# Kernel optimization log

Measured on AMD Instinct MI355X. Metric: run time of the kernel, lower is better.

## Reference

```python
import jax, jax.numpy as jnp
import numpy as np

# Each of the 16 real-valued binary logic gates g_i(a,b) is multilinear in (a,b):
# g_i(a,b) = c0 + c1*a + c2*b + c3*a*b. Rows below are [c0, c1, c2, c3] for gates 0..15
# (false, a&b, a&~b, a, ~a&b, b, xor, or, nor, xnor, ~b, a|~b, ~a, ~a|b, nand, true).
_GATE_COEFFS = np.array([
    [0.0,  0.0,  0.0,  0.0],   # 0: False
    [0.0,  0.0,  0.0,  1.0],   # 1: a AND b
    [0.0,  1.0,  0.0, -1.0],   # 2: a AND NOT b
    [0.0,  1.0,  0.0,  0.0],   # 3: a
    [0.0,  0.0,  1.0, -1.0],   # 4: NOT a AND b
    [0.0,  0.0,  1.0,  0.0],   # 5: b
    [0.0,  1.0,  1.0, -2.0],   # 6: a XOR b
    [0.0,  1.0,  1.0, -1.0],   # 7: a OR b
    [1.0, -1.0, -1.0,  1.0],   # 8: NOR
    [1.0, -1.0, -1.0,  2.0],   # 9: XNOR
    [1.0,  0.0, -1.0,  0.0],   # 10: NOT b
    [1.0,  0.0, -1.0,  1.0],   # 11: a OR NOT b
    [1.0, -1.0,  0.0,  0.0],   # 12: NOT a
    [1.0, -1.0,  0.0,  1.0],   # 13: NOT a OR b
    [1.0,  0.0,  0.0, -1.0],   # 14: NAND
    [1.0,  0.0,  0.0,  0.0],   # 15: True
], dtype=np.float32)

BATCH, IN_DIM, OUT_DIM = 4096, 16384, 16384

def setup_inputs() -> dict:
    key = jax.random.key(0)
    k1, k2, k3, k4 = jax.random.split(key, 4)
    x = jax.random.uniform(k1, (BATCH, IN_DIM), dtype=jnp.float32)
    weights = jax.random.normal(k2, (OUT_DIM, 16), dtype=jnp.float32)
    # get_connections('random'): randperm(2*out_dim) % in_dim -> uniform indices in [0, in_dim)
    a_idx = jax.random.randint(k3, (OUT_DIM,), 0, IN_DIM, dtype=jnp.int64)
    b_idx = jax.random.randint(k4, (OUT_DIM,), 0, IN_DIM, dtype=jnp.int64)
    return {"x": x, "weights": weights, "a_idx": a_idx, "b_idx": b_idx}

def reference(x, weights, a_idx, b_idx):
    # softmax over the 16 gate logits (per output neuron)
    w = jax.nn.softmax(weights, axis=-1).astype(x.dtype)          # [out, 16]
    # collapse 16 gates into 4 multilinear coefficients: k = w @ M  -> [out, 4]
    k = w @ jnp.asarray(_GATE_COEFFS, dtype=x.dtype)
    a = x[:, a_idx]                                               # [batch, out] gather
    b = x[:, b_idx]                                               # [batch, out] gather
    # out[n, y] = k0[y] + k1[y]*a + k2[y]*b + k3[y]*a*b
    return k[:, 0] + k[:, 1] * a + k[:, 2] * b + k[:, 3] * (a * b)
```

## Files before the change

kernel.cpp:

```cpp
#include <hip/hip_runtime.h>


__device__ __constant__ float GC[16][4] = {
    {0.f, 0.f, 0.f, 0.f},  {0.f, 0.f, 0.f, 1.f},
    {0.f, 1.f, 0.f, -1.f}, {0.f, 1.f, 0.f, 0.f},
    {0.f, 0.f, 1.f, -1.f}, {0.f, 0.f, 1.f, 0.f},
    {0.f, 1.f, 1.f, -2.f}, {0.f, 1.f, 1.f, -1.f},
    {1.f, -1.f, -1.f, 1.f},{1.f, -1.f, -1.f, 2.f},
    {1.f, 0.f, -1.f, 0.f}, {1.f, 0.f, -1.f, 1.f},
    {1.f, -1.f, 0.f, 0.f}, {1.f, -1.f, 0.f, 1.f},
    {1.f, 0.f, 0.f, -1.f}, {1.f, 0.f, 0.f, 0.f}};

__global__ void meta_kernel(const float* __restrict__ weights,
                            const int* __restrict__ a_idx,
                            const int* __restrict__ b_idx,
                            float4* __restrict__ k_out,
                            int2* __restrict__ idx_out, int out_dim) {
    int c = blockIdx.x * blockDim.x + threadIdx.x;
    if (c >= out_dim) return;
    const float4* wr = (const float4*)(weights + (size_t)c * 16);
    float4 q0 = wr[0], q1 = wr[1], q2 = wr[2], q3 = wr[3];
    float w[16] = {q0.x, q0.y, q0.z, q0.w, q1.x, q1.y, q1.z, q1.w,
                   q2.x, q2.y, q2.z, q2.w, q3.x, q3.y, q3.z, q3.w};
    float m = w[0];
#pragma unroll
    for (int i = 1; i < 16; ++i) m = fmaxf(m, w[i]);
    float S = 0.f, s0 = 0.f, s1 = 0.f, s2 = 0.f, s3 = 0.f;
#pragma unroll
    for (int i = 0; i < 16; ++i) {
        float e = expf(w[i] - m);
        S += e;
        s0 = fmaf(e, GC[i][0], s0);
        s1 = fmaf(e, GC[i][1], s1);
        s2 = fmaf(e, GC[i][2], s2);
        s3 = fmaf(e, GC[i][3], s3);
    }
    float inv = 1.f / S;
    k_out[c] = make_float4(s0 * inv, s1 * inv, s2 * inv, s3 * inv);
    idx_out[c] = make_int2(a_idx[c], b_idx[c]);
}

__global__ __launch_bounds__(512) void logic_main_kernel(
    const float* __restrict__ x, const float4* __restrict__ k_meta,
    const int2* __restrict__ idx_meta, float* __restrict__ out,
    int in_dim, int out_dim) {
    __shared__ float rowbuf[16384];
    const int row = blockIdx.x;
    const float4* src = (const float4*)(x + (size_t)row * in_dim);
    float4* dst = (float4*)rowbuf;
    const int n4in = in_dim >> 2;
    for (int i = threadIdx.x; i < n4in; i += 512) dst[i] = src[i];
    __syncthreads();

    float4* orow = (float4*)(out + (size_t)row * out_dim);
    const int n4out = out_dim >> 2;
    for (int q = threadIdx.x; q < n4out; q += 512) {
        const int c = q << 2;
        int2 ab0 = idx_meta[c + 0];
        int2 ab1 = idx_meta[c + 1];
        int2 ab2 = idx_meta[c + 2];
        int2 ab3 = idx_meta[c + 3];
        float4 k0 = k_meta[c + 0];
        float4 k1 = k_meta[c + 1];
        float4 k2 = k_meta[c + 2];
        float4 k3 = k_meta[c + 3];
        float a0 = rowbuf[ab0.x], b0 = rowbuf[ab0.y];
        float a1 = rowbuf[ab1.x], b1 = rowbuf[ab1.y];
        float a2 = rowbuf[ab2.x], b2 = rowbuf[ab2.y];
        float a3 = rowbuf[ab3.x], b3 = rowbuf[ab3.y];
        float4 r;
        r.x = fmaf(k0.w, a0 * b0, fmaf(k0.z, b0, fmaf(k0.y, a0, k0.x)));
        r.y = fmaf(k1.w, a1 * b1, fmaf(k1.z, b1, fmaf(k1.y, a1, k1.x)));
        r.z = fmaf(k2.w, a2 * b2, fmaf(k2.z, b2, fmaf(k2.y, a2, k2.x)));
        r.w = fmaf(k3.w, a3 * b3, fmaf(k3.z, b3, fmaf(k3.y, a3, k3.x)));
        orow[q] = r;
    }
}

__global__ void fallback_kernel(const float* __restrict__ x,
                                const float* __restrict__ weights,
                                const int* __restrict__ a_idx,
                                const int* __restrict__ b_idx,
                                float* __restrict__ out, long long total,
                                int in_dim, int out_dim) {
    long long stride = (long long)gridDim.x * blockDim.x;
    for (long long t = (long long)blockIdx.x * blockDim.x + threadIdx.x;
         t < total; t += stride) {
        int c = (int)(t % out_dim);
        long long row = t / out_dim;
        const float* wr = weights + (size_t)c * 16;
        float m = wr[0];
#pragma unroll
        for (int i = 1; i < 16; ++i) m = fmaxf(m, wr[i]);
        float S = 0.f, s0 = 0.f, s1 = 0.f, s2 = 0.f, s3 = 0.f;
#pragma unroll
        for (int i = 0; i < 16; ++i) {
            float e = expf(wr[i] - m);
            S += e;
            s0 = fmaf(e, GC[i][0], s0);
            s1 = fmaf(e, GC[i][1], s1);
            s2 = fmaf(e, GC[i][2], s2);
            s3 = fmaf(e, GC[i][3], s3);
        }
        float inv = 1.f / S;
        float a = x[row * (size_t)in_dim + a_idx[c]];
        float b = x[row * (size_t)in_dim + b_idx[c]];
        out[t] = fmaf(s3 * inv, a * b,
                      fmaf(s2 * inv, b, fmaf(s1 * inv, a, s0 * inv)));
    }
}

extern "C" void kernel_launch(void* const* d_in, const int* in_sizes, int n_in,
                              void* d_out, int out_size, void* d_ws,
                              size_t ws_size, hipStream_t stream) {
    const float* x = (const float*)d_in[0];
    const float* weights = (const float*)d_in[1];
    const int* a_idx = (const int*)d_in[2];
    const int* b_idx = (const int*)d_in[3];
    float* out = (float*)d_out;

    const int out_dim = in_sizes[2];
    const int batch = out_size / out_dim;
    const int in_dim = in_sizes[0] / batch;

    const size_t k_bytes = (size_t)out_dim * sizeof(float4);
    const size_t idx_bytes = (size_t)out_dim * sizeof(int2);

    const bool ok = ws_size >= k_bytes + idx_bytes && in_dim <= 16384 &&
                    (in_dim % 4) == 0 && (out_dim % 4) == 0;
    if (ok) {
        float4* k_meta = (float4*)d_ws;
        int2* idx_meta = (int2*)((char*)d_ws + k_bytes);
        meta_kernel<<<(out_dim + 255) / 256, 256, 0, stream>>>(
            weights, a_idx, b_idx, k_meta, idx_meta, out_dim);
        logic_main_kernel<<<batch, 512, 0, stream>>>(x, k_meta, idx_meta, out,
                                                     in_dim, out_dim);
    } else {
        long long total = (long long)batch * out_dim;
        fallback_kernel<<<4096, 256, 0, stream>>>(x, weights, a_idx, b_idx,
                                                  out, total, in_dim, out_dim);
    }
}
```

Before: 540.7 us.

## Add multi-row double-buffered async-LDS kernel with SoA metadata and streaming stores

Adds a specialised path for the 16384x16384 shape. Each 1024-thread block handles 8 batch rows and double-buffers x rows in LDS using global_load_lds async copies, so the next row loads while the current one is computed. The gather indices stay in registers across rows, the coefficients move to a structure-of-arrays layout for coalesced float4 loads, and outputs use nontemporal stores. The 128KB LDS footprint limits each CU to one block. Correctness depends on the async copies finishing before the barriers.

Result: faster. 482.6 us (-10.7%).

```diff
diff --git a/kernel.cpp b/kernel.cpp
--- a/kernel.cpp
+++ b/kernel.cpp
@@ -1,5 +1,7 @@
 #include <hip/hip_runtime.h>
 
+
+typedef float f32x4 __attribute__((ext_vector_type(4)));
 
 __device__ __constant__ float GC[16][4] = {
     {0.f, 0.f, 0.f, 0.f},  {0.f, 0.f, 0.f, 1.f},
@@ -11,70 +13,174 @@
     {1.f, -1.f, 0.f, 0.f}, {1.f, -1.f, 0.f, 1.f},
     {1.f, 0.f, 0.f, -1.f}, {1.f, 0.f, 0.f, 0.f}};
 
+#define ASYNC_COPY_16B(gsrc, ldst)                                        \
+  __builtin_amdgcn_global_load_lds(                                       \
+      (const __attribute__((address_space(1))) unsigned int*)(gsrc),      \
+      (__attribute__((address_space(3))) unsigned int*)(ldst), 16, 0, 0)
+
+__device__ __forceinline__ void softmax_k(const float* __restrict__ wrow,
+                                          float& k0, float& k1, float& k2,
+                                          float& k3) {
+  const float4* wr = (const float4*)wrow;
+  float4 q0 = wr[0], q1 = wr[1], q2 = wr[2], q3 = wr[3];
+  float w[16] = {q0.x, q0.y, q0.z, q0.w, q1.x, q1.y, q1.z, q1.w,
+                 q2.x, q2.y, q2.z, q2.w, q3.x, q3.y, q3.z, q3.w};
+  float m = w[0];
+#pragma unroll
+  for (int i = 1; i < 16; ++i) m = fmaxf(m, w[i]);
+  float S = 0.f, s0 = 0.f, s1 = 0.f, s2 = 0.f, s3 = 0.f;
+#pragma unroll
+  for (int i = 0; i < 16; ++i) {
+    float e = expf(w[i] - m);
+    S += e;
+    s0 = fmaf(e, GC[i][0], s0);
+    s1 = fmaf(e, GC[i][1], s1);
+    s2 = fmaf(e, GC[i][2], s2);
+    s3 = fmaf(e, GC[i][3], s3);
+  }
+  float inv = 1.f / S;
+  k0 = s0 * inv;
+  k1 = s1 * inv;
+  k2 = s2 * inv;
+  k3 = s3 * inv;
+}
+
+__global__ void meta_soa_kernel(const float* __restrict__ weights,
+                                const int* __restrict__ a_idx,
+                                const int* __restrict__ b_idx,
+                                float* __restrict__ k0, float* __restrict__ k1,
+                                float* __restrict__ k2, float* __restrict__ k3,
+                                int* __restrict__ ai, int* __restrict__ bi,
+                                int out_dim) {
+  int c = blockIdx.x * blockDim.x + threadIdx.x;
+  if (c >= out_dim) return;
+  float a, b, d, e;
+  softmax_k(weights + (size_t)c * 16, a, b, d, e);
+  k0[c] = a;
+  k1[c] = b;
+  k2[c] = d;
+  k3[c] = e;
+  ai[c] = a_idx[c];
+  bi[c] = b_idx[c];
+}
+
+__global__ __launch_bounds__(1024, 4) void logic_fast_kernel(
+    const float* __restrict__ x, const float* __restrict__ k0v,
+    const float* __restrict__ k1v, const float* __restrict__ k2v,
+    const float* __restrict__ k3v, const int* __restrict__ aiv,
+    const int* __restrict__ biv, float* __restrict__ out) {
+  constexpr int IN = 16384;
+  constexpr int OUT = 16384;
+  constexpr int R = 8;
+  __shared__ float buf[2][IN];
+
+  const int tid = threadIdx.x;
+  const int lane = tid & 63;
+  const int wv = tid >> 6;
+  const size_t row0 = (size_t)blockIdx.x * R;
+
+  int4 Am[4], Bm[4];
+#pragma unroll
+  for (int i = 0; i < 4; ++i) {
+    Am[i] = ((const int4*)aiv)[tid + i * 1024];
+    Bm[i] = ((const int4*)biv)[tid + i * 1024];
+  }
+
+  {
+    const float* src = x + row0 * IN;
+#pragma unroll
+    for (int s = 0; s < 4; ++s) {
+      const int chunk = wv + s * 16;
+      ASYNC_COPY_16B(src + chunk * 256 + lane * 4, &buf[0][chunk * 256]);
+    }
+  }
+  __syncthreads();
+
+  for (int r = 0; r < R; ++r) {
+    if (r + 1 < R) {
+      const float* src = x + (row0 + r + 1) * IN;
+#pragma unroll
+      for (int s = 0; s < 4; ++s) {
+        const int chunk = wv + s * 16;
+        ASYNC_COPY_16B(src + chunk * 256 + lane * 4,
+                       &buf[(r + 1) & 1][chunk * 256]);
+      }
+    }
+
+    const float* rb = buf[r & 1];
+    f32x4* orow = (f32x4*)(out + (row0 + r) * OUT);
+#pragma unroll
+    for (int i = 0; i < 4; ++i) {
+      const int q = tid + i * 1024;
+      const float4 K0 = ((const float4*)k0v)[q];
+      const float4 K1 = ((const float4*)k1v)[q];
+      const float4 K2 = ((const float4*)k2v)[q];
+      const float4 K3 = ((const float4*)k3v)[q];
+      const int4 A = Am[i];
+      const int4 B = Bm[i];
+      float a0 = rb[A.x], b0 = rb[B.x];
+      float a1 = rb[A.y], b1 = rb[B.y];
+      float a2 = rb[A.z], b2 = rb[B.z];
+      float a3 = rb[A.w], b3 = rb[B.w];
+      f32x4 rr;
+      rr.x = fmaf(K3.x, a0 * b0, fmaf(K2.x, b0, fmaf(K1.x, a0, K0.x)));
+      rr.y = fmaf(K3.y, a1 * b1, fmaf(K2.y, b1, fmaf(K1.y, a1, K0.y)));
+      rr.z = fmaf(K3.z, a2 * b2, fmaf(K2.z, b2, fmaf(K1.z, a2, K0.z)));
+      rr.w = fmaf(K3.w, a3 * b3, fmaf(K2.w, b3, fmaf(K1.w, a3, K0.w)));
+      __builtin_nontemporal_store(rr, &orow[q]);
+    }
+    __syncthreads();
+  }
+}
+
 __global__ void meta_kernel(const float* __restrict__ weights,
                             const int* __restrict__ a_idx,
                             const int* __restrict__ b_idx,
                             float4* __restrict__ k_out,
                             int2* __restrict__ idx_out, int out_dim) {
-    int c = blockIdx.x * blockDim.x + threadIdx.x;
-    if (c >= out_dim) return;
-    const float4* wr = (const float4*)(weights + (size_t)c * 16);
-    float4 q0 = wr[0], q1 = wr[1], q2 = wr[2], q3 = wr[3];
-    float w[16] = {q0.x, q0.y, q0.z, q0.w, q1.x, q1.y, q1.z, q1.w,
-                   q2.x, q2.y, q2.z, q2.w, q3.x, q3.y, q3.z, q3.w};
-    float m = w[0];
-#pragma unroll
-    for (int i = 1; i < 16; ++i) m = fmaxf(m, w[i]);
-    float S = 0.f, s0 = 0.f, s1 = 0.f, s2 = 0.f, s3 = 0.f;
-#pragma unroll
-    for (int i = 0; i < 16; ++i) {
-        float e = expf(w[i] - m);
-        S += e;
-        s0 = fmaf(e, GC[i][0], s0);
-        s1 = fmaf(e, GC[i][1], s1);
-        s2 = fmaf(e, GC[i][2], s2);
-        s3 = fmaf(e, GC[i][3], s3);
-    }
-    float inv = 1.f / S;
-    k_out[c] = make_float4(s0 * inv, s1 * inv, s2 * inv, s3 * inv);
-    idx_out[c] = make_int2(a_idx[c], b_idx[c]);
+  int c = blockIdx.x * blockDim.x + threadIdx.x;
+  if (c >= out_dim) return;
+  float a, b, d, e;
+  softmax_k(weights + (size_t)c * 16, a, b, d, e);
+  k_out[c] = make_float4(a, b, d, e);
+  idx_out[c] = make_int2(a_idx[c], b_idx[c]);
 }
 
 __global__ __launch_bounds__(512) void logic_main_kernel(
     const float* __restrict__ x, const float4* __restrict__ k_meta,
     const int2* __restrict__ idx_meta, float* __restrict__ out,
     int in_dim, int out_dim) {
-    __shared__ float rowbuf[16384];
-    const int row = blockIdx.x;
-    const float4* src = (const float4*)(x + (size_t)row * in_dim);
-    float4* dst = (float4*)rowbuf;
-    const int n4in = in_dim >> 2;
-    for (int i = threadIdx.x; i < n4in; i += 512) dst[i] = src[i];
-    __syncthreads();
-
-    float4* orow = (float4*)(out + (size_t)row * out_dim);
-    const int n4out = out_dim >> 2;
-    for (int q = threadIdx.x; q < n4out; q += 512) {
-        const int c = q << 2;
-        int2 ab0 = idx_meta[c + 0];
-        int2 ab1 = idx_meta[c + 1];
-        int2 ab2 = idx_meta[c + 2];
-        int2 ab3 = idx_meta[c + 3];
-        float4 k0 = k_meta[c + 0];
-        float4 k1 = k_meta[c + 1];
-        float4 k2 = k_meta[c + 2];
-        float4 k3 = k_meta[c + 3];
-        float a0 = rowbuf[ab0.x], b0 = rowbuf[ab0.y];
-        float a1 = rowbuf[ab1.x], b1 = rowbuf[ab1.y];
-        float a2 = rowbuf[ab2.x], b2 = rowbuf[ab2.y];
-        float a3 = rowbuf[ab3.x], b3 = rowbuf[ab3.y];
-        float4 r;
-        r.x = fmaf(k0.w, a0 * b0, fmaf(k0.z, b0, fmaf(k0.y, a0, k0.x)));
-        r.y = fmaf(k1.w, a1 * b1, fmaf(k1.z, b1, fmaf(k1.y, a1, k1.x)));
-        r.z = fmaf(k2.w, a2 * b2, fmaf(k2.z, b2, fmaf(k2.y, a2, k2.x)));
-        r.w = fmaf(k3.w, a3 * b3, fmaf(k3.z, b3, fmaf(k3.y, a3, k3.x)));
-        orow[q] = r;
-    }
+  __shared__ float rowbuf[16384];
+  const int row = blockIdx.x;
+  const float4* src = (const float4*)(x + (size_t)row * in_dim);
+  float4* dst = (float4*)rowbuf;
+  const int n4in = in_dim >> 2;
+  for (int i = threadIdx.x; i < n4in; i += 512) dst[i] = src[i];
+  __syncthreads();
+
+  float4* orow = (float4*)(out + (size_t)row * out_dim);
+  const int n4out = out_dim >> 2;
+  for (int q = threadIdx.x; q < n4out; q += 512) {
+    const int c = q << 2;
+    int2 ab0 = idx_meta[c + 0];
+    int2 ab1 = idx_meta[c + 1];
+    int2 ab2 = idx_meta[c + 2];
+    int2 ab3 = idx_meta[c + 3];
+    float4 k0 = k_meta[c + 0];
+    float4 k1 = k_meta[c + 1];
+    float4 k2 = k_meta[c + 2];
+    float4 k3 = k_meta[c + 3];
+    float a0 = rowbuf[ab0.x], b0 = rowbuf[ab0.y];
+    float a1 = rowbuf[ab1.x], b1 = rowbuf[ab1.y];
+    float a2 = rowbuf[ab2.x], b2 = rowbuf[ab2.y];
+    float a3 = rowbuf[ab3.x], b3 = rowbuf[ab3.y];
+    float4 r;
+    r.x = fmaf(k0.w, a0 * b0, fmaf(k0.z, b0, fmaf(k0.y, a0, k0.x)));
+    r.y = fmaf(k1.w, a1 * b1, fmaf(k1.z, b1, fmaf(k1.y, a1, k1.x)));
+    r.z = fmaf(k2.w, a2 * b2, fmaf(k2.z, b2, fmaf(k2.y, a2, k2.x)));
+    r.w = fmaf(k3.w, a3 * b3, fmaf(k3.z, b3, fmaf(k3.y, a3, k3.x)));
+    orow[q] = r;
+  }
 }
 
 __global__ void fallback_kernel(const float* __restrict__ x,
@@ -83,61 +189,64 @@
                                 const int* __restrict__ b_idx,
                                 float* __restrict__ out, long long total,
                                 int in_dim, int out_dim) {
-    long long stride = (long long)gridDim.x * blockDim.x;
-    for (long long t = (long long)blockIdx.x * blockDim.x + threadIdx.x;
-         t < total; t += stride) {
-        int c = (int)(t % out_dim);
-        long long row = t / out_dim;
-        const float* wr = weights + (size_t)c * 16;
-        float m = wr[0];
-#pragma unroll
-        for (int i = 1; i < 16; ++i) m = fmaxf(m, wr[i]);
-        float S = 0.f, s0 = 0.f, s1 = 0.f, s2 = 0.f, s3 = 0.f;
-#pragma unroll
-        for (int i = 0; i < 16; ++i) {
-            float e = expf(wr[i] - m);
-            S += e;
-            s0 = fmaf(e, GC[i][0], s0);
-            s1 = fmaf(e, GC[i][1], s1);
-            s2 = fmaf(e, GC[i][2], s2);
-            s3 = fmaf(e, GC[i][3], s3);
-        }
-        float inv = 1.f / S;
-        float a = x[row * (size_t)in_dim + a_idx[c]];
-        float b = x[row * (size_t)in_dim + b_idx[c]];
-        out[t] = fmaf(s3 * inv, a * b,
-                      fmaf(s2 * inv, b, fmaf(s1 * inv, a, s0 * inv)));
-    }
+  long long stride = (long long)gridDim.x * blockDim.x;
+  for (long long t = (long long)blockIdx.x * blockDim.x + threadIdx.x;
+       t < total; t += stride) {
+    int c = (int)(t % out_dim);
+    long long row = t / out_dim;
+    float k0, k1, k2, k3;
+    softmax_k(weights + (size_t)c * 16, k0, k1, k2, k3);
+    float a = x[row * (size_t)in_dim + a_idx[c]];
+    float b = x[row * (size_t)in_dim + b_idx[c]];
+    out[t] = fmaf(k3, a * b, fmaf(k2, b, fmaf(k1, a, k0)));
+  }
 }
 
 extern "C" void kernel_launch(void* const* d_in, const int* in_sizes, int n_in,
                               void* d_out, int out_size, void* d_ws,
                               size_t ws_size, hipStream_t stream) {
-    const float* x = (const float*)d_in[0];
-    const float* weights = (const float*)d_in[1];
-    const int* a_idx = (const int*)d_in[2];
-    const int* b_idx = (const int*)d_in[3];
-    float* out = (float*)d_out;
-
-    const int out_dim = in_sizes[2];
-    const int batch = out_size / out_dim;
-    const int in_dim = in_sizes[0] / batch;
-
-    const size_t k_bytes = (size_t)out_dim * sizeof(float4);
-    const size_t idx_bytes = (size_t)out_dim * sizeof(int2);
-
-    const bool ok = ws_size >= k_bytes + idx_bytes && in_dim <= 16384 &&
-                    (in_dim % 4) == 0 && (out_dim % 4) == 0;
-    if (ok) {
-        float4* k_meta = (float4*)d_ws;
-        int2* idx_meta = (int2*)((char*)d_ws + k_bytes);
-        meta_kernel<<<(out_dim + 255) / 256, 256, 0, stream>>>(
-            weights, a_idx, b_idx, k_meta, idx_meta, out_dim);
-        logic_main_kernel<<<batch, 512, 0, stream>>>(x, k_meta, idx_meta, out,
-                                                     in_dim, out_dim);
-    } else {
-        long long total = (long long)batch * out_dim;
-        fallback_kernel<<<4096, 256, 0, stream>>>(x, weights, a_idx, b_idx,
-                                                  out, total, in_dim, out_dim);
-    }
-}
+  const float* x = (const float*)d_in[0];
+  const float* weights = (const float*)d_in[1];
+  const int* a_idx = (const int*)d_in[2];
+  const int* b_idx = (const int*)d_in[3];
+  float* out = (float*)d_out;
+
+  const int out_dim = in_sizes[2];
+  const int batch = out_size / out_dim;
+  const int in_dim = in_sizes[0] / batch;
+
+  const size_t soa_bytes = (size_t)out_dim * 24;
+  const bool fast = (in_dim == 16384) && (out_dim == 16384) &&
+                    (batch % 8 == 0) && ws_size >= soa_bytes;
+
+  if (fast) {
+    float* k0 = (float*)d_ws;
+    float* k1 = k0 + out_dim;
+    float* k2 = k1 + out_dim;
+    float* k3 = k2 + out_dim;
+    int* ai = (int*)(k3 + out_dim);
+    int* bi = ai + out_dim;
+    meta_soa_kernel<<<(out_dim + 255) / 256, 256, 0, stream>>>(
+        weights, a_idx, b_idx, k0, k1, k2, k3, ai, bi, out_dim);
+    logic_fast_kernel<<<batch / 8, 1024, 0, stream>>>(x, k0, k1, k2, k3, ai,
+                                                      bi, out);
+    return;
+  }
+
+  const size_t k_bytes = (size_t)out_dim * sizeof(float4);
+  const size_t idx_bytes = (size_t)out_dim * sizeof(int2);
+  const bool ok = ws_size >= k_bytes + idx_bytes && in_dim <= 16384 &&
+                  (in_dim % 4) == 0 && (out_dim % 4) == 0;
+  if (ok) {
+    float4* k_meta = (float4*)d_ws;
+    int2* idx_meta = (int2*)((char*)d_ws + k_bytes);
+    meta_kernel<<<(out_dim + 255) / 256, 256, 0, stream>>>(
+        weights, a_idx, b_idx, k_meta, idx_meta, out_dim);
+    logic_main_kernel<<<batch, 512, 0, stream>>>(x, k_meta, idx_meta, out,
+                                                 in_dim, out_dim);
+  } else {
+    long long total = (long long)batch * out_dim;
+    fallback_kernel<<<4096, 256, 0, stream>>>(x, weights, a_idx, b_idx, out,
+                                              total, in_dim, out_dim);
+  }
+}
```
